# Performance work log

Hardware: AMD Instinct MI355X
Metric: run time of the kernel (lower is better)

## Reference

```python
import jax, jax.numpy as jnp
import numpy as np

B, A, S, IN, H, OUT, T = 32768, 10, 50, 6, 64, 2, 60


def _p(key, shape, scale=0.1):
    return (jax.random.normal(key, shape) * scale).astype(jnp.float32)


def setup_inputs() -> dict:
    key = jax.random.key(0)
    ks = jax.random.split(key, 20)
    inp = {
        'history': jax.random.normal(ks[0], (B, A, S, IN), dtype=jnp.float32),
        # encoder layer 0 (IN->H) and layer 1 (H->H); PyTorch gate order i,f,g,o
        'enc_Wih0': _p(ks[1], (4 * H, IN)), 'enc_Whh0': _p(ks[2], (4 * H, H)),
        'enc_bih0': _p(ks[3], (4 * H,)),    'enc_bhh0': _p(ks[4], (4 * H,)),
        'enc_Wih1': _p(ks[5], (4 * H, H)),  'enc_Whh1': _p(ks[6], (4 * H, H)),
        'enc_bih1': _p(ks[7], (4 * H,)),    'enc_bhh1': _p(ks[8], (4 * H,)),
        # decoder layer 0 (OUT->H) and layer 1 (H->H)
        'dec_Wih0': _p(ks[9], (4 * H, OUT)), 'dec_Whh0': _p(ks[10], (4 * H, H)),
        'dec_bih0': _p(ks[11], (4 * H,)),    'dec_bhh0': _p(ks[12], (4 * H,)),
        'dec_Wih1': _p(ks[13], (4 * H, H)),  'dec_Whh1': _p(ks[14], (4 * H, H)),
        'dec_bih1': _p(ks[15], (4 * H,)),    'dec_bhh1': _p(ks[16], (4 * H,)),
        'lin_W': _p(ks[17], (OUT, H)), 'lin_b': _p(ks[18], (OUT,)),
        'start_token': _p(ks[19], (1, 1, OUT)),
    }
    return inp


def _cell(x, h, c, Wih, Whh, bih, bhh):
    g = x @ Wih.T + h @ Whh.T + (bih + bhh)
    i, f, gg, o = jnp.split(g, 4, axis=-1)
    c2 = jax.nn.sigmoid(f) * c + jax.nn.sigmoid(i) * jnp.tanh(gg)
    h2 = jax.nn.sigmoid(o) * jnp.tanh(c2)
    return h2, c2


def reference(history, enc_Wih0, enc_Whh0, enc_bih0, enc_bhh0,
              enc_Wih1, enc_Whh1, enc_bih1, enc_bhh1,
              dec_Wih0, dec_Whh0, dec_bih0, dec_bhh0,
              dec_Wih1, dec_Whh1, dec_bih1, dec_bhh1,
              lin_W, lin_b, start_token):
    ego = history[:, 0]                     # [B, S, IN]
    b = ego.shape[0]
    z = jnp.zeros((b, H), dtype=ego.dtype)

    def enc_step(carry, xt):
        h0, c0, h1, c1 = carry
        h0, c0 = _cell(xt, h0, c0, enc_Wih0, enc_Whh0, enc_bih0, enc_bhh0)
        h1, c1 = _cell(h0, h1, c1, enc_Wih1, enc_Whh1, enc_bih1, enc_bhh1)
        return (h0, c0, h1, c1), None

    (h0, c0, h1, c1), _ = jax.lax.scan(enc_step, (z, z, z, z),
                                       jnp.swapaxes(ego, 0, 1))  # time-major [S,B,IN]

    start = jnp.broadcast_to(start_token[0], (b, start_token.shape[2]))  # [B, OUT]

    def dec_step(carry, _):
        h0, c0, h1, c1, inp = carry
        h0, c0 = _cell(inp, h0, c0, dec_Wih0, dec_Whh0, dec_bih0, dec_bhh0)
        h1, c1 = _cell(h0, h1, c1, dec_Wih1, dec_Whh1, dec_bih1, dec_bhh1)
        out = h1 @ lin_W.T + lin_b           # [B, OUT]
        return (h0, c0, h1, c1, out), out

    _, preds = jax.lax.scan(dec_step, (h0, c0, h1, c1, start), None, length=T)
    return jnp.swapaxes(preds, 0, 1)         # [B, T, OUT]
```

## Files before the change

kernel.cpp:

```cpp
#include <hip/hip_runtime.h>
#include <stdint.h>

typedef float f32x4 __attribute__((ext_vector_type(4)));
typedef __bf16 bf16x8 __attribute__((ext_vector_type(8)));

#define SEQ 50
#define TDEC 60

static __device__ __forceinline__ float ex2(float x) { return __builtin_amdgcn_exp2f(x); }
static __device__ __forceinline__ float frcp_(float x) { return __builtin_amdgcn_rcpf(x); }
static __device__ __forceinline__ __bf16 bfc(float x) { return (__bf16)x; }

__global__ __launch_bounds__(256, 1) void lstm_s2s(
    const float* __restrict__ hist,
    const float* __restrict__ eWih0, const float* __restrict__ eWhh0,
    const float* __restrict__ ebih0, const float* __restrict__ ebhh0,
    const float* __restrict__ eWih1, const float* __restrict__ eWhh1,
    const float* __restrict__ ebih1, const float* __restrict__ ebhh1,
    const float* __restrict__ dWih0, const float* __restrict__ dWhh0,
    const float* __restrict__ dbih0, const float* __restrict__ dbhh0,
    const float* __restrict__ dWih1, const float* __restrict__ dWhh1,
    const float* __restrict__ dbih1, const float* __restrict__ dbhh1,
    const float* __restrict__ linW, const float* __restrict__ linb,
    const float* __restrict__ stok,
    float* __restrict__ out)
{
  __shared__ __bf16 xbuf[SEQ * 64 * 8];
  __shared__ __bf16 hb0[4096];
  __shared__ __bf16 hb1[4096];
  __shared__ __bf16 obuf[64 * 8];

  const int tid = threadIdx.x;
  const int lane = tid & 63;
  const int w = tid >> 6;
  const int c = lane & 15;
  const int q = lane >> 4;
  const long rowbase = (long)blockIdx.x * 64;

  bf16x8 zfrag;
#pragma unroll
  for (int j = 0; j < 8; ++j) zfrag[j] = (__bf16)0.0f;

  {
    const float* eg = hist + rowbase * 3000;
    for (int i = tid; i < 64 * 300; i += 256) {
      int row = i / 300;
      int o = i - row * 300;
      int t = o / 6;
      int k = o - t * 6;
      xbuf[(t * 64 + row) * 8 + k] = bfc(eg[row * 3000 + o]);
    }
    for (int i = tid; i < 64 * SEQ; i += 256) {
      xbuf[i * 8 + 6] = (__bf16)0.0f;
      xbuf[i * 8 + 7] = (__bf16)0.0f;
    }
    for (int i = tid; i < 2048; i += 256) {
      ((unsigned int*)hb0)[i] = 0u;
      ((unsigned int*)hb1)[i] = 0u;
    }
  }

  const float GS[4] = {-1.442695041f, -1.442695041f, 2.885390082f, -1.442695041f};

  bf16x8 wxL0[4];
  bf16x8 whL0[4][2], wxL1[4][2], whL1[4][2];
  float bs0[4], bs1[4];

  auto loadFull = [&](const float* W, bf16x8 (*dst)[2]) {
#pragma unroll
    for (int g = 0; g < 4; ++g)
#pragma unroll
      for (int kc = 0; kc < 2; ++kc) {
        const float* p = W + ((g * 4 + w) * 16 + c) * 64 + kc * 32 + q * 8;
        f32x4 a = *(const f32x4*)p;
        f32x4 b = *(const f32x4*)(p + 4);
        bf16x8 f;
        f[0] = bfc(GS[g] * a[0]); f[1] = bfc(GS[g] * a[1]);
        f[2] = bfc(GS[g] * a[2]); f[3] = bfc(GS[g] * a[3]);
        f[4] = bfc(GS[g] * b[0]); f[5] = bfc(GS[g] * b[1]);
        f[6] = bfc(GS[g] * b[2]); f[7] = bfc(GS[g] * b[3]);
        dst[g][kc] = f;
      }
  };
  auto loadPad = [&](const float* W, int Kin, bf16x8* dst) {
#pragma unroll
    for (int g = 0; g < 4; ++g) {
      bf16x8 f = zfrag;
      if (q == 0) {
        const float* p = W + ((g * 4 + w) * 16 + c) * Kin;
        for (int j = 0; j < Kin; ++j) f[j] = bfc(GS[g] * p[j]);
      }
      dst[g] = f;
    }
  };
  auto loadBias = [&](const float* bi, const float* bh, float* bs) {
#pragma unroll
    for (int g = 0; g < 4; ++g) {
      int n = g * 64 + w * 16 + c;
      bs[g] = GS[g] * (bi[n] + bh[n]);
    }
  };

  const int u = w * 16 + c;
  const int wconst = (u >> 5) * 2048 + ((u >> 3) & 3) * 128 + q * 32 + (u & 7);

  float cs0[16], cs1[16];
#pragma unroll
  for (int i = 0; i < 16; ++i) { cs0[i] = 0.0f; cs1[i] = 0.0f; }

  auto epilogue = [&](f32x4 (*acc)[4], __bf16* hb, float* cs) {
    __syncthreads();
#pragma unroll
    for (int mt = 0; mt < 4; ++mt)
#pragma unroll
      for (int r = 0; r < 4; ++r) {
        float eI = ex2(acc[0][mt][r]);
        float eF = ex2(acc[1][mt][r]);
        float eG = ex2(acc[2][mt][r]);
        float eO = ex2(acc[3][mt][r]);
        float cc = cs[mt * 4 + r];
        float c2 = frcp_(1.0f + eF) * cc +
                   (eG - 1.0f) * frcp_((1.0f + eI) * (eG + 1.0f));
        float eC = ex2(2.885390082f * c2);
        float h2 = (eC - 1.0f) * frcp_((1.0f + eO) * (eC + 1.0f));
        cs[mt * 4 + r] = c2;
        hb[wconst + mt * 512 + r * 8] = bfc(h2);
      }
    __syncthreads();
  };

  auto cellF = [&](const __bf16* xsrc, const bf16x8 (*wx)[2], const bf16x8 (*wh)[2],
                   __bf16* hb, const float* bs, float* cs) {
    f32x4 acc[4][4];
#pragma unroll
    for (int g = 0; g < 4; ++g) {
      float b = bs[g];
#pragma unroll
      for (int mt = 0; mt < 4; ++mt) {
        acc[g][mt][0] = b; acc[g][mt][1] = b; acc[g][mt][2] = b; acc[g][mt][3] = b;
      }
    }
#pragma unroll
    for (int kc = 0; kc < 2; ++kc)
#pragma unroll
      for (int mt = 0; mt < 4; ++mt) {
        bf16x8 xf = *(const bf16x8*)(xsrc + (kc * 4 + mt) * 512 + lane * 8);
#pragma unroll
        for (int g = 0; g < 4; ++g)
          acc[g][mt] = __builtin_amdgcn_mfma_f32_16x16x32_bf16(xf, wx[g][kc], acc[g][mt], 0, 0, 0);
      }
#pragma unroll
    for (int kc = 0; kc < 2; ++kc)
#pragma unroll
      for (int mt = 0; mt < 4; ++mt) {
        bf16x8 hf = *(const bf16x8*)(hb + (kc * 4 + mt) * 512 + lane * 8);
#pragma unroll
        for (int g = 0; g < 4; ++g)
          acc[g][mt] = __builtin_amdgcn_mfma_f32_16x16x32_bf16(hf, wh[g][kc], acc[g][mt], 0, 0, 0);
      }
    epilogue(acc, hb, cs);
  };

  auto cellP = [&](const __bf16* xsrc, int t, const bf16x8* wxp, const bf16x8 (*wh)[2],
                   __bf16* hb, const float* bs, float* cs) {
    f32x4 acc[4][4];
#pragma unroll
    for (int g = 0; g < 4; ++g) {
      float b = bs[g];
#pragma unroll
      for (int mt = 0; mt < 4; ++mt) {
        acc[g][mt][0] = b; acc[g][mt][1] = b; acc[g][mt][2] = b; acc[g][mt][3] = b;
      }
    }
#pragma unroll
    for (int mt = 0; mt < 4; ++mt) {
      bf16x8 xf = zfrag;
      if (q == 0) xf = *(const bf16x8*)(xsrc + (t * 64 + mt * 16 + c) * 8);
#pragma unroll
      for (int g = 0; g < 4; ++g)
        acc[g][mt] = __builtin_amdgcn_mfma_f32_16x16x32_bf16(xf, wxp[g], acc[g][mt], 0, 0, 0);
    }
#pragma unroll
    for (int kc = 0; kc < 2; ++kc)
#pragma unroll
      for (int mt = 0; mt < 4; ++mt) {
        bf16x8 hf = *(const bf16x8*)(hb + (kc * 4 + mt) * 512 + lane * 8);
#pragma unroll
        for (int g = 0; g < 4; ++g)
          acc[g][mt] = __builtin_amdgcn_mfma_f32_16x16x32_bf16(hf, wh[g][kc], acc[g][mt], 0, 0, 0);
      }
    epilogue(acc, hb, cs);
  };

  loadPad(eWih0, 6, wxL0);
  loadFull(eWhh0, whL0);
  loadFull(eWih1, wxL1);
  loadFull(eWhh1, whL1);
  loadBias(ebih0, ebhh0, bs0);
  loadBias(ebih1, ebhh1, bs1);

  __syncthreads();

#pragma unroll 1
  for (int t = 0; t < SEQ; ++t) {
    cellP(xbuf, t, wxL0, whL0, hb0, bs0, cs0);
    cellF(hb0, wxL1, whL1, hb1, bs1, cs1);
  }

  loadPad(dWih0, 2, wxL0);
  loadFull(dWhh0, whL0);
  loadFull(dWih1, wxL1);
  loadFull(dWhh1, whL1);
  loadBias(dbih0, dbhh0, bs0);
  loadBias(dbih1, dbhh1, bs1);

  bf16x8 wlin[2];
#pragma unroll
  for (int kc = 0; kc < 2; ++kc) {
    bf16x8 f = zfrag;
    if (c < 2) {
      const float* p = linW + c * 64 + kc * 32 + q * 8;
#pragma unroll
      for (int j = 0; j < 8; ++j) f[j] = bfc(p[j]);
    }
    wlin[kc] = f;
  }
  const float lb = (c < 2) ? linb[c] : 0.0f;

  {
    float s0 = stok[0], s1 = stok[1];
    for (int i = tid; i < 64; i += 256) {
      obuf[i * 8 + 0] = bfc(s0);
      obuf[i * 8 + 1] = bfc(s1);
#pragma unroll
      for (int j = 2; j < 8; ++j) obuf[i * 8 + j] = (__bf16)0.0f;
    }
  }
  __syncthreads();

#pragma unroll 1
  for (int t = 0; t < TDEC; ++t) {
    cellP(obuf, 0, wxL0, whL0, hb0, bs0, cs0);
    cellF(hb0, wxL1, whL1, hb1, bs1, cs1);
    {
      f32x4 oa;
      oa[0] = lb; oa[1] = lb; oa[2] = lb; oa[3] = lb;
#pragma unroll
      for (int kc = 0; kc < 2; ++kc) {
        bf16x8 hf = *(const bf16x8*)(hb1 + (kc * 4 + w) * 512 + lane * 8);
        oa = __builtin_amdgcn_mfma_f32_16x16x32_bf16(hf, wlin[kc], oa, 0, 0, 0);
      }
      if (c < 2) {
#pragma unroll
        for (int r = 0; r < 4; ++r) {
          int row = w * 16 + q * 4 + r;
          float v = oa[r];
          out[(rowbase + row) * 120 + t * 2 + c] = v;
          obuf[row * 8 + c] = bfc(v);
        }
      }
    }
    __syncthreads();
  }
}

extern "C" void kernel_launch(void* const* d_in, const int* in_sizes, int n_in,
                              void* d_out, int out_size, void* d_ws, size_t ws_size,
                              hipStream_t stream) {
  (void)in_sizes; (void)n_in; (void)d_ws; (void)ws_size; (void)out_size;
  const float* p[20];
  for (int i = 0; i < 20; ++i) p[i] = (const float*)d_in[i];
  dim3 grid(512), block(256);
  hipLaunchKernelGGL(lstm_s2s, grid, block, 0, stream,
                     p[0], p[1], p[2], p[3], p[4], p[5], p[6], p[7], p[8], p[9],
                     p[10], p[11], p[12], p[13], p[14], p[15], p[16], p[17], p[18], p[19],
                     (float*)d_out);
}
```

Baseline: 1.236 ms.

## Double-buffer hidden state, chunk input staging, move small weights to LDS for 2 blocks/CU

```diff
diff --git a/kernel.cpp b/kernel.cpp
--- a/kernel.cpp
+++ b/kernel.cpp
@@ -6,12 +6,13 @@
 
 #define SEQ 50
 #define TDEC 60
+#define XCH 10
 
 static __device__ __forceinline__ float ex2(float x) { return __builtin_amdgcn_exp2f(x); }
 static __device__ __forceinline__ float frcp_(float x) { return __builtin_amdgcn_rcpf(x); }
 static __device__ __forceinline__ __bf16 bfc(float x) { return (__bf16)x; }
 
-__global__ __launch_bounds__(256, 1) void lstm_s2s(
+__global__ __launch_bounds__(256, 2) void lstm_s2s(
     const float* __restrict__ hist,
     const float* __restrict__ eWih0, const float* __restrict__ eWhh0,
     const float* __restrict__ ebih0, const float* __restrict__ ebhh0,
@@ -25,10 +26,12 @@
     const float* __restrict__ stok,
     float* __restrict__ out)
 {
-  __shared__ __bf16 xbuf[SEQ * 64 * 8];
-  __shared__ __bf16 hb0[4096];
-  __shared__ __bf16 hb1[4096];
+  __shared__ __bf16 xch[XCH * 64 * 8];
+  __shared__ __bf16 hb0[2][4096];
+  __shared__ __bf16 hb1[2][4096];
   __shared__ __bf16 obuf[64 * 8];
+  __shared__ __bf16 wx0s[4 * 4 * 64 * 8];
+  __shared__ __bf16 wlc[128];
 
   const int tid = threadIdx.x;
   const int lane = tid & 63;
@@ -36,35 +39,18 @@
   const int c = lane & 15;
   const int q = lane >> 4;
   const long rowbase = (long)blockIdx.x * 64;
+  const float* eg = hist + rowbase * 3000;
 
   bf16x8 zfrag;
 #pragma unroll
   for (int j = 0; j < 8; ++j) zfrag[j] = (__bf16)0.0f;
-
-  {
-    const float* eg = hist + rowbase * 3000;
-    for (int i = tid; i < 64 * 300; i += 256) {
-      int row = i / 300;
-      int o = i - row * 300;
-      int t = o / 6;
-      int k = o - t * 6;
-      xbuf[(t * 64 + row) * 8 + k] = bfc(eg[row * 3000 + o]);
-    }
-    for (int i = tid; i < 64 * SEQ; i += 256) {
-      xbuf[i * 8 + 6] = (__bf16)0.0f;
-      xbuf[i * 8 + 7] = (__bf16)0.0f;
-    }
-    for (int i = tid; i < 2048; i += 256) {
-      ((unsigned int*)hb0)[i] = 0u;
-      ((unsigned int*)hb1)[i] = 0u;
-    }
-  }
+  f32x4 zero4;
+  zero4[0] = 0.f; zero4[1] = 0.f; zero4[2] = 0.f; zero4[3] = 0.f;
 
   const float GS[4] = {-1.442695041f, -1.442695041f, 2.885390082f, -1.442695041f};
 
-  bf16x8 wxL0[4];
   bf16x8 whL0[4][2], wxL1[4][2], whL1[4][2];
-  float bs0[4], bs1[4];
+  float bs1[4];
 
   auto loadFull = [&](const float* W, bf16x8 (*dst)[2]) {
 #pragma unroll
@@ -82,17 +68,6 @@
         dst[g][kc] = f;
       }
   };
-  auto loadPad = [&](const float* W, int Kin, bf16x8* dst) {
-#pragma unroll
-    for (int g = 0; g < 4; ++g) {
-      bf16x8 f = zfrag;
-      if (q == 0) {
-        const float* p = W + ((g * 4 + w) * 16 + c) * Kin;
-        for (int j = 0; j < Kin; ++j) f[j] = bfc(GS[g] * p[j]);
-      }
-      dst[g] = f;
-    }
-  };
   auto loadBias = [&](const float* bi, const float* bh, float* bs) {
 #pragma unroll
     for (int g = 0; g < 4; ++g) {
@@ -100,6 +75,38 @@
       bs[g] = GS[g] * (bi[n] + bh[n]);
     }
   };
+  auto stageWx0 = [&](const float* W, int Kin, const float* bi, const float* bh) {
+    for (int s = tid; s < 1024; s += 256) {
+      int w2 = s >> 8;
+      int g = (s >> 6) & 3;
+      int ln = s & 63;
+      int cc = ln & 15, qq = ln >> 4;
+      float gs = (g == 2) ? 2.885390082f : -1.442695041f;
+      __bf16* dst = wx0s + s * 8;
+      int row = (g * 4 + w2) * 16 + cc;
+      if (qq == 0) {
+        for (int j = 0; j < 8; ++j) {
+          float v = 0.0f;
+          if (j < Kin) v = W[row * Kin + j];
+          else if (j == 6) v = bi[row] + bh[row];
+          dst[j] = bfc(gs * v);
+        }
+      } else {
+        for (int j = 0; j < 8; ++j) dst[j] = (__bf16)0.0f;
+      }
+    }
+  };
+  auto stageX = [&](int t0) {
+    for (int i = tid; i < XCH * 64 * 8; i += 256) {
+      int k = i & 7;
+      int row = (i >> 3) & 63;
+      int tl = i >> 9;
+      float v;
+      if (k < 6) v = eg[row * 3000 + (t0 + tl) * 6 + k];
+      else v = (k == 6) ? 1.0f : 0.0f;
+      xch[i] = bfc(v);
+    }
+  };
 
   const int u = w * 16 + c;
   const int wconst = (u >> 5) * 2048 + ((u >> 3) & 3) * 128 + q * 32 + (u & 7);
@@ -108,8 +115,7 @@
 #pragma unroll
   for (int i = 0; i < 16; ++i) { cs0[i] = 0.0f; cs1[i] = 0.0f; }
 
-  auto epilogue = [&](f32x4 (*acc)[4], __bf16* hb, float* cs) {
-    __syncthreads();
+  auto epilogue = [&](f32x4 (*acc)[4], __bf16* hnxt, float* cs) {
 #pragma unroll
     for (int mt = 0; mt < 4; ++mt)
 #pragma unroll
@@ -124,131 +130,131 @@
         float eC = ex2(2.885390082f * c2);
         float h2 = (eC - 1.0f) * frcp_((1.0f + eO) * (eC + 1.0f));
         cs[mt * 4 + r] = c2;
-        hb[wconst + mt * 512 + r * 8] = bfc(h2);
+        hnxt[wconst + mt * 512 + r * 8] = bfc(h2);
       }
     __syncthreads();
   };
 
-  auto cellF = [&](const __bf16* xsrc, const bf16x8 (*wx)[2], const bf16x8 (*wh)[2],
-                   __bf16* hb, const float* bs, float* cs) {
+  auto cellP = [&](const __bf16* xsrc, const __bf16* hcur, __bf16* hnxt, float* cs) {
+    bf16x8 wxf[4];
+#pragma unroll
+    for (int g = 0; g < 4; ++g)
+      wxf[g] = *(const bf16x8*)(wx0s + (w * 256 + g * 64 + lane) * 8);
     f32x4 acc[4][4];
-#pragma unroll
-    for (int g = 0; g < 4; ++g) {
-      float b = bs[g];
-#pragma unroll
-      for (int mt = 0; mt < 4; ++mt) {
-        acc[g][mt][0] = b; acc[g][mt][1] = b; acc[g][mt][2] = b; acc[g][mt][3] = b;
-      }
-    }
-#pragma unroll
-    for (int kc = 0; kc < 2; ++kc)
-#pragma unroll
-      for (int mt = 0; mt < 4; ++mt) {
-        bf16x8 xf = *(const bf16x8*)(xsrc + (kc * 4 + mt) * 512 + lane * 8);
-#pragma unroll
-        for (int g = 0; g < 4; ++g)
-          acc[g][mt] = __builtin_amdgcn_mfma_f32_16x16x32_bf16(xf, wx[g][kc], acc[g][mt], 0, 0, 0);
-      }
-#pragma unroll
-    for (int kc = 0; kc < 2; ++kc)
-#pragma unroll
-      for (int mt = 0; mt < 4; ++mt) {
-        bf16x8 hf = *(const bf16x8*)(hb + (kc * 4 + mt) * 512 + lane * 8);
-#pragma unroll
-        for (int g = 0; g < 4; ++g)
-          acc[g][mt] = __builtin_amdgcn_mfma_f32_16x16x32_bf16(hf, wh[g][kc], acc[g][mt], 0, 0, 0);
-      }
-    epilogue(acc, hb, cs);
-  };
-
-  auto cellP = [&](const __bf16* xsrc, int t, const bf16x8* wxp, const bf16x8 (*wh)[2],
-                   __bf16* hb, const float* bs, float* cs) {
-    f32x4 acc[4][4];
-#pragma unroll
-    for (int g = 0; g < 4; ++g) {
-      float b = bs[g];
-#pragma unroll
-      for (int mt = 0; mt < 4; ++mt) {
-        acc[g][mt][0] = b; acc[g][mt][1] = b; acc[g][mt][2] = b; acc[g][mt][3] = b;
-      }
-    }
 #pragma unroll
     for (int mt = 0; mt < 4; ++mt) {
       bf16x8 xf = zfrag;
-      if (q == 0) xf = *(const bf16x8*)(xsrc + (t * 64 + mt * 16 + c) * 8);
+      if (q == 0) xf = *(const bf16x8*)(xsrc + (mt * 16 + c) * 8);
 #pragma unroll
       for (int g = 0; g < 4; ++g)
-        acc[g][mt] = __builtin_amdgcn_mfma_f32_16x16x32_bf16(xf, wxp[g], acc[g][mt], 0, 0, 0);
+        acc[g][mt] = __builtin_amdgcn_mfma_f32_16x16x32_bf16(xf, wxf[g], zero4, 0, 0, 0),
+        (void)0;
     }
 #pragma unroll
     for (int kc = 0; kc < 2; ++kc)
 #pragma unroll
       for (int mt = 0; mt < 4; ++mt) {
-        bf16x8 hf = *(const bf16x8*)(hb + (kc * 4 + mt) * 512 + lane * 8);
+        bf16x8 hf = *(const bf16x8*)(hcur + (kc * 4 + mt) * 512 + lane * 8);
 #pragma unroll
         for (int g = 0; g < 4; ++g)
-          acc[g][mt] = __builtin_amdgcn_mfma_f32_16x16x32_bf16(hf, wh[g][kc], acc[g][mt], 0, 0, 0);
-      }
-    epilogue(acc, hb, cs);
-  };
-
-  loadPad(eWih0, 6, wxL0);
+          acc[g][mt] = __builtin_amdgcn_mfma_f32_16x16x32_bf16(hf, whL0[g][kc], acc[g][mt], 0, 0, 0);
+      }
+    epilogue(acc, hnxt, cs);
+  };
+
+  auto cellF = [&](const __bf16* xcur, const __bf16* hcur, __bf16* hnxt, float* cs) {
+    f32x4 acc[4][4];
+#pragma unroll
+    for (int g = 0; g < 4; ++g) {
+      float b = bs1[g];
+#pragma unroll
+      for (int mt = 0; mt < 4; ++mt) {
+        acc[g][mt][0] = b; acc[g][mt][1] = b; acc[g][mt][2] = b; acc[g][mt][3] = b;
+      }
+    }
+#pragma unroll
+    for (int kc = 0; kc < 2; ++kc)
+#pragma unroll
+      for (int mt = 0; mt < 4; ++mt) {
+        bf16x8 xf = *(const bf16x8*)(xcur + (kc * 4 + mt) * 512 + lane * 8);
+#pragma unroll
+        for (int g = 0; g < 4; ++g)
+          acc[g][mt] = __builtin_amdgcn_mfma_f32_16x16x32_bf16(xf, wxL1[g][kc], acc[g][mt], 0, 0, 0);
+      }
+#pragma unroll
+    for (int kc = 0; kc < 2; ++kc)
+#pragma unroll
+      for (int mt = 0; mt < 4; ++mt) {
+        bf16x8 hf = *(const bf16x8*)(hcur + (kc * 4 + mt) * 512 + lane * 8);
+#pragma unroll
+        for (int g = 0; g < 4; ++g)
+          acc[g][mt] = __builtin_amdgcn_mfma_f32_16x16x32_bf16(hf, whL1[g][kc], acc[g][mt], 0, 0, 0);
+      }
+    epilogue(acc, hnxt, cs);
+  };
+
+  for (int i = tid; i < 2048; i += 256) {
+    ((unsigned int*)hb0[0])[i] = 0u;
+    ((unsigned int*)hb1[0])[i] = 0u;
+  }
+
+  stageWx0(eWih0, 6, ebih0, ebhh0);
   loadFull(eWhh0, whL0);
   loadFull(eWih1, wxL1);
   loadFull(eWhh1, whL1);
-  loadBias(ebih0, ebhh0, bs0);
   loadBias(ebih1, ebhh1, bs1);
 
-  __syncthreads();
-
+  int pc = 0;
 #pragma unroll 1
   for (int t = 0; t < SEQ; ++t) {
-    cellP(xbuf, t, wxL0, whL0, hb0, bs0, cs0);
-    cellF(hb0, wxL1, whL1, hb1, bs1, cs1);
-  }
-
-  loadPad(dWih0, 2, wxL0);
+    if ((t % XCH) == 0) {
+      stageX(t);
+      __syncthreads();
+    }
+    cellP(xch + (t % XCH) * 512, hb0[pc], hb0[pc ^ 1], cs0);
+    cellF(hb0[pc ^ 1], hb1[pc], hb1[pc ^ 1], cs1);
+    pc ^= 1;
+  }
+
+  stageWx0(dWih0, 2, dbih0, dbhh0);
   loadFull(dWhh0, whL0);
   loadFull(dWih1, wxL1);
   loadFull(dWhh1, whL1);
-  loadBias(dbih0, dbhh0, bs0);
   loadBias(dbih1, dbhh1, bs1);
 
-  bf16x8 wlin[2];
-#pragma unroll
-  for (int kc = 0; kc < 2; ++kc) {
-    bf16x8 f = zfrag;
-    if (c < 2) {
-      const float* p = linW + c * 64 + kc * 32 + q * 8;
-#pragma unroll
-      for (int j = 0; j < 8; ++j) f[j] = bfc(p[j]);
-    }
-    wlin[kc] = f;
+  for (int i = tid; i < 128; i += 256) {
+    int kc = i >> 6, cc = (i >> 5) & 1, kk = i & 31;
+    wlc[(kc * 2 + cc) * 32 + kk] = bfc(linW[cc * 64 + kc * 32 + kk]);
   }
   const float lb = (c < 2) ? linb[c] : 0.0f;
-
   {
     float s0 = stok[0], s1 = stok[1];
     for (int i = tid; i < 64; i += 256) {
       obuf[i * 8 + 0] = bfc(s0);
       obuf[i * 8 + 1] = bfc(s1);
-#pragma unroll
-      for (int j = 2; j < 8; ++j) obuf[i * 8 + j] = (__bf16)0.0f;
+      obuf[i * 8 + 2] = (__bf16)0.0f;
+      obuf[i * 8 + 3] = (__bf16)0.0f;
+      obuf[i * 8 + 4] = (__bf16)0.0f;
+      obuf[i * 8 + 5] = (__bf16)0.0f;
+      obuf[i * 8 + 6] = (__bf16)1.0f;
+      obuf[i * 8 + 7] = (__bf16)0.0f;
     }
   }
   __syncthreads();
 
 #pragma unroll 1
   for (int t = 0; t < TDEC; ++t) {
-    cellP(obuf, 0, wxL0, whL0, hb0, bs0, cs0);
-    cellF(hb0, wxL1, whL1, hb1, bs1, cs1);
+    cellP(obuf, hb0[pc], hb0[pc ^ 1], cs0);
+    cellF(hb0[pc ^ 1], hb1[pc], hb1[pc ^ 1], cs1);
     {
       f32x4 oa;
       oa[0] = lb; oa[1] = lb; oa[2] = lb; oa[3] = lb;
 #pragma unroll
       for (int kc = 0; kc < 2; ++kc) {
-        bf16x8 hf = *(const bf16x8*)(hb1 + (kc * 4 + w) * 512 + lane * 8);
-        oa = __builtin_amdgcn_mfma_f32_16x16x32_bf16(hf, wlin[kc], oa, 0, 0, 0);
+        bf16x8 hf = *(const bf16x8*)(hb1[pc ^ 1] + (kc * 4 + w) * 512 + lane * 8);
+        bf16x8 wf = zfrag;
+        if (c < 2) wf = *(const bf16x8*)(wlc + (kc * 2 + c) * 32 + q * 8);
+        oa = __builtin_amdgcn_mfma_f32_16x16x32_bf16(hf, wf, oa, 0, 0, 0);
       }
       if (c < 2) {
 #pragma unroll
@@ -261,6 +267,7 @@
       }
     }
     __syncthreads();
+    pc ^= 1;
   }
 }
 
```

Result: faster. 1.165 ms (-5.8%).
